# Kernel tuning notes

Measured on AMD Instinct MI355X. Metric: run time of the kernel, lower is better.

Reference implementation:

```python
import jax, jax.numpy as jnp
import numpy as np

B, N, C, H = 2, 2048, 1024, 16
D = C // H  # head_dim = 64


def _rope_freqs(n, d_half, theta=10000.0):
    inv = 1.0 / (theta ** (np.arange(0, d_half, dtype=np.float32) / d_half))
    ang = np.arange(n, dtype=np.float32)[:, None] * inv[None, :]
    return jnp.asarray(np.cos(ang)), jnp.asarray(np.sin(ang))


def setup_inputs() -> dict:
    key = jax.random.key(0)
    ks = jax.random.split(key, 5)
    cos, sin = _rope_freqs(N, D // 2)
    s = 0.02
    return {
        "x": jax.random.normal(ks[0], (B, N, C), jnp.float32),
        "w_qkv": jax.random.normal(ks[1], (3 * C, C), jnp.float32) * s,
        "b_qkv": jnp.zeros((3 * C,), jnp.float32),
        "w_proj": jax.random.normal(ks[2], (C, C), jnp.float32) * s,
        "b_proj": jnp.zeros((C,), jnp.float32),
        "freqs_cos": cos,
        "freqs_sin": sin,
    }


def _apply_rope(t, cos, sin):
    # t: (B, H, N, D); consecutive pairs (even, odd) form complex numbers,
    # matching torch.view_as_complex on reshape(..., D//2, 2).
    te = t[..., 0::2]
    to = t[..., 1::2]
    cos = cos[None, None, :, :]  # (1,1,N,D//2)
    sin = sin[None, None, :, :]
    oe = te * cos - to * sin
    oo = te * sin + to * cos
    return jnp.stack([oe, oo], axis=-1).reshape(t.shape)


def reference(x, w_qkv, b_qkv, w_proj, b_proj, freqs_cos, freqs_sin):
    b, n, c = x.shape
    qkv = x @ w_qkv.T + b_qkv                      # (B,N,3C)
    qkv = qkv.reshape(b, n, 3, H, D).transpose(2, 0, 3, 1, 4)  # (3,B,H,N,D)
    q, k, v = qkv[0], qkv[1], qkv[2]
    q = _apply_rope(q, freqs_cos, freqs_sin)
    k = _apply_rope(k, freqs_cos, freqs_sin)
    scale = 1.0 / jnp.sqrt(jnp.asarray(D, x.dtype))
    scores = jnp.einsum("bhqd,bhkd->bhqk", q, k) * scale
    attn = jax.nn.softmax(scores, axis=-1)
    out = jnp.einsum("bhqk,bhkd->bhqd", attn, v)   # (B,H,N,D)
    out = out.transpose(0, 2, 1, 3).reshape(b, n, c)
    return out @ w_proj.T + b_proj
```

## Files before the change

### kernel.cpp

```cpp
#include <hip/hip_runtime.h>
#include <hip/hip_bf16.h>
#include <stdint.h>

#define BB 2
#define NN 2048
#define CC 1024
#define HH 16
#define DD 64
#define C3 3072

typedef __attribute__((ext_vector_type(8))) short bf16x8;
typedef __attribute__((ext_vector_type(4))) short bf16x4;
typedef __attribute__((ext_vector_type(4))) float f32x4;
typedef __attribute__((ext_vector_type(16))) float f32x16;
typedef __attribute__((ext_vector_type(4))) unsigned short ushort4_t;

__device__ __forceinline__ unsigned short f2bf(float f) {
  union { float f; unsigned u; } v; v.f = f;
  unsigned r = v.u + 0x7FFFu + ((v.u >> 16) & 1u);
  return (unsigned short)(r >> 16);
}

#if __has_builtin(__builtin_amdgcn_exp2f)
#define EXP2(x) __builtin_amdgcn_exp2f(x)
#else
#define EXP2(x) exp2f(x)
#endif

__device__ __forceinline__ unsigned pack_bf2(float a, float b) {
  union { float f; unsigned u; } ua, ub; ua.f = a; ub.f = b;
#if __has_builtin(__builtin_amdgcn_perm)
  return __builtin_amdgcn_perm(ub.u, ua.u, 0x07060302u);
#else
  return (ua.u >> 16) | (ub.u & 0xFFFF0000u);
#endif
}

#define QSCALE 0.18033688f

#define GLDS(g, l) __builtin_amdgcn_global_load_lds( \
    (const __attribute__((address_space(1))) void*)(g), \
    (__attribute__((address_space(3))) void*)(l), 16, 0, 0)

__global__ __launch_bounds__(256) void k_cvt(
    const float* __restrict__ x, const float* __restrict__ wq,
    const float* __restrict__ wp,
    unsigned short* __restrict__ xb, unsigned short* __restrict__ wqb,
    unsigned short* __restrict__ wpb)
{
  int blk = blockIdx.x;
  const float* s; unsigned short* d; int i;
  if (blk < 4096)      { s = x;  d = xb;  i = blk * 256 + threadIdx.x; }
  else if (blk < 7168) { s = wq; d = wqb; i = (blk - 4096) * 256 + threadIdx.x; }
  else                 { s = wp; d = wpb; i = (blk - 7168) * 256 + threadIdx.x; }
  float4 v = ((const float4*)s)[i];
  ushort4_t o;
  o.x = f2bf(v.x); o.y = f2bf(v.y); o.z = f2bf(v.z); o.w = f2bf(v.w);
  ((ushort4_t*)d)[i] = o;
}

__global__ __launch_bounds__(256) void k_gemm_qkv(
    const unsigned short* __restrict__ A, const unsigned short* __restrict__ Bt,
    const float* __restrict__ bias,
    const float* __restrict__ cosb, const float* __restrict__ sinb,
    unsigned short* __restrict__ Qg, unsigned short* __restrict__ Kg,
    unsigned short* __restrict__ Vt)
{
  __shared__ __align__(16) unsigned short Sh[16384];
  const int tid  = threadIdx.x;
  const int lane = tid & 63;
  const int wave = tid >> 6;
  const int bm = blockIdx.y * 128;
  const int bn = blockIdx.x * 128;
  const int wm = (wave >> 1) * 64;
  const int wn = (wave & 1) * 64;
  const int frow = lane & 15;
  const int fk   = (lane >> 4) * 8;
  const int K = 1024;
  const int NIT = K / 32;

  f32x4 acc[4][4] = {};

  const int row0 = tid >> 2, cc0 = tid & 3;
  const int row1 = row0 + 64;
  const unsigned short* Arow0 = A  + (size_t)(bm + row0) * K + cc0 * 8;
  const unsigned short* Arow1 = A  + (size_t)(bm + row1) * K + cc0 * 8;
  const unsigned short* Brow0 = Bt + (size_t)(bn + row0) * K + cc0 * 8;
  const unsigned short* Brow1 = Bt + (size_t)(bn + row1) * K + cc0 * 8;

  GLDS(Arow0, Sh + (size_t)tid * 8);
  GLDS(Brow0, Sh + 4096 + (size_t)tid * 8);
  GLDS(Arow1, Sh + (size_t)(tid + 256) * 8);
  GLDS(Brow1, Sh + 4096 + (size_t)(tid + 256) * 8);

  for (int it = 0; it < NIT; ++it) {
    const int p = it & 1;
    const unsigned short* As = Sh + p * 8192;
    const unsigned short* Bs = As + 4096;
    __syncthreads();

    if (it + 1 < NIT) {
      const int k1 = (it + 1) * 32;
      unsigned short* An = Sh + (1 - p) * 8192;
      GLDS(Arow0 + k1, An + (size_t)tid * 8);
      GLDS(Brow0 + k1, An + 4096 + (size_t)tid * 8);
      GLDS(Arow1 + k1, An + (size_t)(tid + 256) * 8);
      GLDS(Brow1 + k1, An + 4096 + (size_t)(tid + 256) * 8);
    }

    bf16x8 af[4], bfr[4];
#pragma unroll
    for (int t = 0; t < 4; ++t) {
      af[t]  = *(const bf16x8*)(As + (wm + t * 16 + frow) * 32 + fk);
      bfr[t] = *(const bf16x8*)(Bs + (wn + t * 16 + frow) * 32 + fk);
    }
#pragma unroll
    for (int mt = 0; mt < 4; ++mt)
#pragma unroll
      for (int nt = 0; nt < 4; ++nt)
        acc[mt][nt] = __builtin_amdgcn_mfma_f32_16x16x32_bf16(af[mt], bfr[nt], acc[mt][nt], 0, 0, 0);
  }
  __syncthreads();

  const int er0  = (lane >> 4) * 4;
  const int ecol = lane & 15;
  const int region = bn >> 10;
  const int gcol0 = bn + wn;
  const int h  = (gcol0 >> 6) & 15;
  const int rowg0 = bm + wm;
  const int b  = rowg0 >> 11;
  const int n0 = rowg0 & (NN - 1);
  unsigned short* wt = Sh + wave * 4096;

#pragma unroll
  for (int nt = 0; nt < 4; ++nt) {
    const int c64 = nt * 16 + ecol;
    const float bv = bias[gcol0 + c64];
    const int ii  = c64 >> 1;
#pragma unroll
    for (int mt = 0; mt < 4; ++mt)
#pragma unroll
      for (int r = 0; r < 4; ++r) {
        const int ml = mt * 16 + er0 + r;
        const int n  = n0 + ml;
        float v = acc[mt][nt][r] + bv;
        float vp = __shfl_xor(v, 1, 64);
        if (region == 2) {
          wt[c64 * 64 + ((((ml >> 3) ^ (c64 & 7)) << 3) | (ml & 7))] = f2bf(v);
        } else {
          float cth = cosb[n * 32 + ii], sth = sinb[n * 32 + ii];
          float ov = (c64 & 1) ? (vp * sth + v * cth)
                               : (v * cth - vp * sth);
          if (region == 0) ov *= QSCALE;
          wt[ml * 64 + ((((c64 >> 3) ^ (ml & 7)) << 3) | (c64 & 7))] = f2bf(ov);
        }
      }
  }

  const int rr = lane >> 3, cc = lane & 7;
  if (region == 2) {
    unsigned short* dst = Vt + (size_t)(b * HH + h) * DD * NN + n0;
    const int q8a = (cc >> 1) * 2;
    const int q8b = q8a + 1;
    const int half = (cc & 1) * 4;
#pragma unroll
    for (int it = 0; it < 8; ++it) {
      int dl = it * 8 + rr;
      union { bf16x4 h[2]; bf16x8 w; } vv;
      vv.h[0] = *(const bf16x4*)(wt + dl * 64 + ((q8a ^ (dl & 7)) << 3) + half);
      vv.h[1] = *(const bf16x4*)(wt + dl * 64 + ((q8b ^ (dl & 7)) << 3) + half);
      *(bf16x8*)(dst + (size_t)dl * NN + cc * 8) = vv.w;
    }
  } else {
    unsigned short* dqk = ((region == 0) ? Qg : Kg) +
                          ((size_t)(b * HH + h) * NN + n0) * DD;
#pragma unroll
    for (int it = 0; it < 8; ++it) {
      int ml = it * 8 + rr;
      bf16x8 vv = *(const bf16x8*)(wt + ml * 64 + ((cc ^ (ml & 7)) << 3));
      *(bf16x8*)(dqk + (size_t)ml * DD + cc * 8) = vv;
    }
  }
}

__global__ __launch_bounds__(256) void k_attn(
    const unsigned short* __restrict__ Qg, const unsigned short* __restrict__ Kg,
    const unsigned short* __restrict__ Vtg, unsigned short* __restrict__ Og)
{
  __shared__ __align__(16) unsigned short Ks[3][64 * 64];
  __shared__ __align__(16) unsigned short Vs[3][64 * 64];

  const int tid  = threadIdx.x;
  const int lane = tid & 63;
  const int wave = tid >> 6;
  const int bh = blockIdx.x >> 4;
  const int qt = blockIdx.x & 15;
  const int q0 = qt * 128 + wave * 32;
  const int l31 = lane & 31;
  const int hi  = lane >> 5;
  const int s7  = l31 & 7;

  const unsigned short* Qb = Qg  + (size_t)bh * NN * DD;
  const unsigned short* Kb = Kg  + (size_t)bh * NN * DD;
  const unsigned short* Vb = Vtg + (size_t)bh * DD * NN;

  int soffB[4];
#pragma unroll
  for (int i = 0; i < 4; ++i)
    soffB[i] = (l31 * 64 + (((2 * i + hi) ^ s7) << 3)) * 2;

  bf16x8 qf[4];
#pragma unroll
  for (int dc = 0; dc < 4; ++dc)
    qf[dc] = *(const bf16x8*)(Qb + (size_t)(q0 + l31) * DD + dc * 16 + hi * 8);

  bf16x8 ones;
#pragma unroll
  for (int i = 0; i < 8; ++i) ones[i] = (short)0x3F80;

  f32x16 oacc[2] = {};
  f32x16 lacc = {};

  const int row0 = tid >> 3, cc0 = tid & 7;
  const int sw0 = (cc0 ^ (row0 & 7)) * 8;

#define STAGE_KV(bf, j) do { \
    GLDS(Kb + (size_t)((j) + row0) * DD + sw0,      Ks[bf] + (size_t)tid * 8); \
    GLDS(Vb + (size_t)row0 * NN + (j) + sw0,        Vs[bf] + (size_t)tid * 8); \
    GLDS(Kb + (size_t)((j) + row0 + 32) * DD + sw0, Ks[bf] + (size_t)(tid + 256) * 8); \
    GLDS(Vb + (size_t)(row0 + 32) * NN + (j) + sw0, Vs[bf] + (size_t)(tid + 256) * 8); \
  } while (0)

  STAGE_KV(0, 0);
  STAGE_KV(1, 64);

  int bc = 0;
  int bs = 2;
  const int NT = NN / 64;

  for (int t = 0; t < NT; ++t) {
    if (t == NT - 1) asm volatile("s_waitcnt vmcnt(0)" ::: "memory");
    else             asm volatile("s_waitcnt vmcnt(4)" ::: "memory");
    __builtin_amdgcn_s_barrier();
    __builtin_amdgcn_sched_barrier(0);

    if (t + 2 < NT) STAGE_KV(bs, (t + 2) * 64);

    const char* KsB = (const char*)Ks[bc];
    const char* VsB = (const char*)Vs[bc];

    f32x16 sacc[2] = {};
    __builtin_amdgcn_s_setprio(1);
#pragma unroll
    for (int T = 0; T < 2; ++T)
#pragma unroll
      for (int dc = 0; dc < 4; ++dc) {
        bf16x8 kf = *(const bf16x8*)(KsB + T * 4096 + soffB[dc]);
        sacc[T] = __builtin_amdgcn_mfma_f32_32x32x16_bf16(kf, qf[dc], sacc[T], 0, 0, 0);
      }
    __builtin_amdgcn_s_setprio(0);

#pragma unroll
    for (int T = 0; T < 2; ++T) {
      unsigned pk[8];
#pragma unroll
      for (int jj = 0; jj < 8; ++jj) {
        float e0 = EXP2(sacc[T][2 * jj]);
        float e1 = EXP2(sacc[T][2 * jj + 1]);
        pk[jj] = pack_bf2(e0, e1);
      }
      union { unsigned u[4]; bf16x8 v; } fa, fb;
      fa.u[0] = pk[0]; fa.u[1] = pk[1]; fa.u[2] = pk[2]; fa.u[3] = pk[3];
      fb.u[0] = pk[4]; fb.u[1] = pk[5]; fb.u[2] = pk[6]; fb.u[3] = pk[7];
      __builtin_amdgcn_s_setprio(1);
#pragma unroll
      for (int dt = 0; dt < 2; ++dt) {
        bf16x8 v0 = *(const bf16x8*)(VsB + dt * 4096 + soffB[2 * T + 0]);
        bf16x8 v1 = *(const bf16x8*)(VsB + dt * 4096 + soffB[2 * T + 1]);
        oacc[dt] = __builtin_amdgcn_mfma_f32_32x32x16_bf16(fa.v, v0, oacc[dt], 0, 0, 0);
        oacc[dt] = __builtin_amdgcn_mfma_f32_32x32x16_bf16(fb.v, v1, oacc[dt], 0, 0, 0);
      }
      lacc = __builtin_amdgcn_mfma_f32_32x32x16_bf16(fa.v, ones, lacc, 0, 0, 0);
      lacc = __builtin_amdgcn_mfma_f32_32x32x16_bf16(fb.v, ones, lacc, 0, 0, 0);
      __builtin_amdgcn_s_setprio(0);
    }

    bc = (bc == 2) ? 0 : bc + 1;
    bs = (bs == 2) ? 0 : bs + 1;
  }
#undef STAGE_KV

  const int b = bh >> 4;
  const int h = bh & 15;
#pragma unroll
  for (int r = 0; r < 16; ++r) {
    const int qr = (r & 3) + 8 * (r >> 2) + 4 * hi;
    const float linv = 1.0f / lacc[r];
    unsigned short* orow = Og + (size_t)(b * NN + q0 + qr) * CC + h * DD + l31;
    orow[0]  = f2bf(oacc[0][r] * linv);
    orow[32] = f2bf(oacc[1][r] * linv);
  }
}

__global__ __launch_bounds__(256) void k_gemm_proj(
    const unsigned short* __restrict__ A, const unsigned short* __restrict__ Bt,
    const float* __restrict__ bias, float* __restrict__ Co)
{
  __shared__ __align__(16) unsigned short As[2][64 * 32];
  __shared__ __align__(16) unsigned short Bs[2][128 * 32];
  const int tid  = threadIdx.x;
  const int lane = tid & 63;
  const int wave = tid >> 6;
  const int bm = blockIdx.y * 64;
  const int bn = blockIdx.x * 128;
  const int wm = (wave >> 1) * 32;
  const int wn = (wave & 1) * 64;
  const int frow = lane & 15;
  const int fk   = (lane >> 4) * 8;
  const int K = 1024;
  const int NIT = K / 32;

  f32x4 acc[2][4] = {};

  const int row0 = tid >> 2, cc0 = tid & 3;
  const unsigned short* Arow  = A  + (size_t)(bm + row0) * K + cc0 * 8;
  const unsigned short* Brow0 = Bt + (size_t)(bn + row0) * K + cc0 * 8;
  const unsigned short* Brow1 = Bt + (size_t)(bn + row0 + 64) * K + cc0 * 8;

  GLDS(Arow,  As[0] + (size_t)tid * 8);
  GLDS(Brow0, Bs[0] + (size_t)tid * 8);
  GLDS(Brow1, Bs[0] + (size_t)(tid + 256) * 8);

  for (int it = 0; it < NIT; ++it) {
    const int p = it & 1;
    __syncthreads();

    if (it + 1 < NIT) {
      const int k1 = (it + 1) * 32;
      GLDS(Arow  + k1, As[1 - p] + (size_t)tid * 8);
      GLDS(Brow0 + k1, Bs[1 - p] + (size_t)tid * 8);
      GLDS(Brow1 + k1, Bs[1 - p] + (size_t)(tid + 256) * 8);
    }

    bf16x8 af[2], bfr[4];
#pragma unroll
    for (int t = 0; t < 2; ++t)
      af[t] = *(const bf16x8*)(As[p] + (wm + t * 16 + frow) * 32 + fk);
#pragma unroll
    for (int t = 0; t < 4; ++t)
      bfr[t] = *(const bf16x8*)(Bs[p] + (wn + t * 16 + frow) * 32 + fk);
#pragma unroll
    for (int mt = 0; mt < 2; ++mt)
#pragma unroll
      for (int nt = 0; nt < 4; ++nt)
        acc[mt][nt] = __builtin_amdgcn_mfma_f32_16x16x32_bf16(af[mt], bfr[nt], acc[mt][nt], 0, 0, 0);
  }

  const int er0  = (lane >> 4) * 4;
  const int ecol = lane & 15;
#pragma unroll
  for (int nt = 0; nt < 4; ++nt) {
    int col = bn + wn + nt * 16 + ecol;
    float bv = bias[col];
#pragma unroll
    for (int mt = 0; mt < 2; ++mt)
#pragma unroll
      for (int r = 0; r < 4; ++r) {
        int rowg = bm + wm + mt * 16 + er0 + r;
        Co[(size_t)rowg * CC + col] = acc[mt][nt][r] + bv;
      }
  }
}

extern "C" void kernel_launch(void* const* d_in, const int* in_sizes, int n_in,
                              void* d_out, int out_size, void* d_ws, size_t ws_size,
                              hipStream_t stream)
{
  const float* x      = (const float*)d_in[0];
  const float* w_qkv  = (const float*)d_in[1];
  const float* b_qkv  = (const float*)d_in[2];
  const float* w_proj = (const float*)d_in[3];
  const float* b_proj = (const float*)d_in[4];
  const float* fcos   = (const float*)d_in[5];
  const float* fsin   = (const float*)d_in[6];
  float* out = (float*)d_out;

  char* ws = (char*)d_ws;
  unsigned short* xb     = (unsigned short*)(ws);
  unsigned short* wqkvb  = (unsigned short*)(ws + 8388608);
  unsigned short* wprojb = (unsigned short*)(ws + 14680064);
  unsigned short* Qb     = (unsigned short*)(ws + 16777216);
  unsigned short* Kb     = (unsigned short*)(ws + 25165824);
  unsigned short* Vtb    = (unsigned short*)(ws + 33554432);
  unsigned short* aob    = (unsigned short*)(ws + 41943040);

  k_cvt<<<8192, 256, 0, stream>>>(x, w_qkv, w_proj, xb, wqkvb, wprojb);

  k_gemm_qkv<<<dim3(24, 32), 256, 0, stream>>>(xb, wqkvb, b_qkv, fcos, fsin,
                                               Qb, Kb, Vtb);

  k_attn<<<512, 256, 0, stream>>>(Qb, Kb, Vtb, aob);

  k_gemm_proj<<<dim3(8, 64), 256, 0, stream>>>(aob, wprojb, b_proj, out);
}
```

Baseline: 205.1 us.

## Restructure attention K/V pipeline into 128-key double-buffered stages

Replaces the triple-buffered 64-key ring with two 128-key stage pairs (four 64-key LDS buffers), prefetching the next 128 keys while computing the current two sub-tiles. It uses one __syncthreads per 128 keys instead of a waitcnt plus barrier per 64 keys, and seeds the score MFMA chain from a zero constant. This halves barrier count but uses more LDS and drains outstanding loads at each barrier, which may reduce overlap and occupancy.

```diff
diff --git a/kernel.cpp b/kernel.cpp
--- a/kernel.cpp
+++ b/kernel.cpp
@@ -187,8 +187,8 @@
     const unsigned short* __restrict__ Qg, const unsigned short* __restrict__ Kg,
     const unsigned short* __restrict__ Vtg, unsigned short* __restrict__ Og)
 {
-  __shared__ __align__(16) unsigned short Ks[3][64 * 64];
-  __shared__ __align__(16) unsigned short Vs[3][64 * 64];
+  __shared__ __align__(16) unsigned short Ks[4][64 * 64];
+  __shared__ __align__(16) unsigned short Vs[4][64 * 64];
 
   const int tid  = threadIdx.x;
   const int lane = tid & 63;
@@ -217,6 +217,7 @@
   bf16x8 ones;
 #pragma unroll
   for (int i = 0; i < 8; ++i) ones[i] = (short)0x3F80;
+  const f32x16 zero16 = {};
 
   f32x16 oacc[2] = {};
   f32x16 lacc = {};
@@ -224,71 +225,73 @@
   const int row0 = tid >> 3, cc0 = tid & 7;
   const int sw0 = (cc0 ^ (row0 & 7)) * 8;
 
-#define STAGE_KV(bf, j) do { \
+#define STAGE64(bf, j) do { \
     GLDS(Kb + (size_t)((j) + row0) * DD + sw0,      Ks[bf] + (size_t)tid * 8); \
     GLDS(Vb + (size_t)row0 * NN + (j) + sw0,        Vs[bf] + (size_t)tid * 8); \
     GLDS(Kb + (size_t)((j) + row0 + 32) * DD + sw0, Ks[bf] + (size_t)(tid + 256) * 8); \
     GLDS(Vb + (size_t)(row0 + 32) * NN + (j) + sw0, Vs[bf] + (size_t)(tid + 256) * 8); \
   } while (0)
 
-  STAGE_KV(0, 0);
-  STAGE_KV(1, 64);
-
-  int bc = 0;
-  int bs = 2;
-  const int NT = NN / 64;
-
+  STAGE64(0, 0);
+  STAGE64(1, 64);
+
+  const int NT = NN / 128;
+#pragma unroll 2
   for (int t = 0; t < NT; ++t) {
-    if (t == NT - 1) asm volatile("s_waitcnt vmcnt(0)" ::: "memory");
-    else             asm volatile("s_waitcnt vmcnt(4)" ::: "memory");
-    __builtin_amdgcn_s_barrier();
-    __builtin_amdgcn_sched_barrier(0);
-
-    if (t + 2 < NT) STAGE_KV(bs, (t + 2) * 64);
-
-    const char* KsB = (const char*)Ks[bc];
-    const char* VsB = (const char*)Vs[bc];
-
-    f32x16 sacc[2] = {};
-    __builtin_amdgcn_s_setprio(1);
-#pragma unroll
-    for (int T = 0; T < 2; ++T)
-#pragma unroll
-      for (int dc = 0; dc < 4; ++dc) {
-        bf16x8 kf = *(const bf16x8*)(KsB + T * 4096 + soffB[dc]);
-        sacc[T] = __builtin_amdgcn_mfma_f32_32x32x16_bf16(kf, qf[dc], sacc[T], 0, 0, 0);
+    const int p = t & 1;
+    __syncthreads();
+
+    if (t + 1 < NT) {
+      STAGE64(2 * (1 - p),     (t + 1) * 128);
+      STAGE64(2 * (1 - p) + 1, (t + 1) * 128 + 64);
+    }
+
+#pragma unroll
+    for (int sub = 0; sub < 2; ++sub) {
+      const char* KsB = (const char*)Ks[2 * p + sub];
+      const char* VsB = (const char*)Vs[2 * p + sub];
+
+      f32x16 sacc[2];
+      __builtin_amdgcn_s_setprio(1);
+#pragma unroll
+      for (int T = 0; T < 2; ++T) {
+        bf16x8 kf0 = *(const bf16x8*)(KsB + T * 4096 + soffB[0]);
+        sacc[T] = __builtin_amdgcn_mfma_f32_32x32x16_bf16(kf0, qf[0], zero16, 0, 0, 0);
+#pragma unroll
+        for (int dc = 1; dc < 4; ++dc) {
+          bf16x8 kf = *(const bf16x8*)(KsB + T * 4096 + soffB[dc]);
+          sacc[T] = __builtin_amdgcn_mfma_f32_32x32x16_bf16(kf, qf[dc], sacc[T], 0, 0, 0);
+        }
       }
-    __builtin_amdgcn_s_setprio(0);
-
-#pragma unroll
-    for (int T = 0; T < 2; ++T) {
-      unsigned pk[8];
-#pragma unroll
-      for (int jj = 0; jj < 8; ++jj) {
-        float e0 = EXP2(sacc[T][2 * jj]);
-        float e1 = EXP2(sacc[T][2 * jj + 1]);
-        pk[jj] = pack_bf2(e0, e1);
+      __builtin_amdgcn_s_setprio(0);
+
+#pragma unroll
+      for (int T = 0; T < 2; ++T) {
+        unsigned pk[8];
+#pragma unroll
+        for (int jj = 0; jj < 8; ++jj) {
+          float e0 = EXP2(sacc[T][2 * jj]);
+          float e1 = EXP2(sacc[T][2 * jj + 1]);
+          pk[jj] = pack_bf2(e0, e1);
+        }
+        union { unsigned u[4]; bf16x8 v; } fa, fb;
+        fa.u[0] = pk[0]; fa.u[1] = pk[1]; fa.u[2] = pk[2]; fa.u[3] = pk[3];
+        fb.u[0] = pk[4]; fb.u[1] = pk[5]; fb.u[2] = pk[6]; fb.u[3] = pk[7];
+        __builtin_amdgcn_s_setprio(1);
+#pragma unroll
+        for (int dt = 0; dt < 2; ++dt) {
+          bf16x8 v0 = *(const bf16x8*)(VsB + dt * 4096 + soffB[2 * T + 0]);
+          bf16x8 v1 = *(const bf16x8*)(VsB + dt * 4096 + soffB[2 * T + 1]);
+          oacc[dt] = __builtin_amdgcn_mfma_f32_32x32x16_bf16(fa.v, v0, oacc[dt], 0, 0, 0);
+          oacc[dt] = __builtin_amdgcn_mfma_f32_32x32x16_bf16(fb.v, v1, oacc[dt], 0, 0, 0);
+        }
+        lacc = __builtin_amdgcn_mfma_f32_32x32x16_bf16(fa.v, ones, lacc, 0, 0, 0);
+        lacc = __builtin_amdgcn_mfma_f32_32x32x16_bf16(fb.v, ones, lacc, 0, 0, 0);
+        __builtin_amdgcn_s_setprio(0);
       }
-      union { unsigned u[4]; bf16x8 v; } fa, fb;
-      fa.u[0] = pk[0]; fa.u[1] = pk[1]; fa.u[2] = pk[2]; fa.u[3] = pk[3];
-      fb.u[0] = pk[4]; fb.u[1] = pk[5]; fb.u[2] = pk[6]; fb.u[3] = pk[7];
-      __builtin_amdgcn_s_setprio(1);
-#pragma unroll
-      for (int dt = 0; dt < 2; ++dt) {
-        bf16x8 v0 = *(const bf16x8*)(VsB + dt * 4096 + soffB[2 * T + 0]);
-        bf16x8 v1 = *(const bf16x8*)(VsB + dt * 4096 + soffB[2 * T + 1]);
-        oacc[dt] = __builtin_amdgcn_mfma_f32_32x32x16_bf16(fa.v, v0, oacc[dt], 0, 0, 0);
-        oacc[dt] = __builtin_amdgcn_mfma_f32_32x32x16_bf16(fb.v, v1, oacc[dt], 0, 0, 0);
-      }
-      lacc = __builtin_amdgcn_mfma_f32_32x32x16_bf16(fa.v, ones, lacc, 0, 0, 0);
-      lacc = __builtin_amdgcn_mfma_f32_32x32x16_bf16(fb.v, ones, lacc, 0, 0, 0);
-      __builtin_amdgcn_s_setprio(0);
-    }
-
-    bc = (bc == 2) ? 0 : bc + 1;
-    bs = (bs == 2) ? 0 : bs + 1;
-  }
-#undef STAGE_KV
+    }
+  }
+#undef STAGE64
 
   const int b = bh >> 4;
   const int h = bh & 15;
```

Result: faster. 199.5 us (-2.7%).
